# Optimization experiments

Hardware: AMD Instinct MI355X
Metric: run time of the kernel (lower is better)

The kernel has to match this reference:

```python
import jax, jax.numpy as jnp
import numpy as np

BATCH, N_IN, N_OUT, K = 32768, 256, 256, 8

def setup_inputs() -> dict:
    key = jax.random.key(0)
    k1, k2, k3 = jax.random.split(key, 3)
    x = jax.random.normal(k1, (BATCH, N_IN), dtype=jnp.float32)
    coef_a = jax.random.normal(k2, (N_OUT, N_IN, K), dtype=jnp.float32)
    coef_b = jax.random.normal(k3, (N_OUT, N_IN, K), dtype=jnp.float32)
    return {"x": x, "coef_a": coef_a, "coef_b": coef_b}

def reference(x, coef_a, coef_b):
    # Each edge (j, i) applies a univariate Fourier series to x[:, i]:
    #   f_ji(t) = sum_k a[j,i,k] * cos((k+1) t) + b[j,i,k] * sin((k+1) t)
    # Output: S[b, j] = sum_i f_ji(x[b, i])  (activation = identity)
    freqs = jnp.arange(1, K + 1, dtype=x.dtype)          # [K]
    phase = x[:, :, None] * freqs                        # [batch, n_in, K]
    S = (jnp.einsum('bik,jik->bj', jnp.cos(phase), coef_a)
         + jnp.einsum('bik,jik->bj', jnp.sin(phase), coef_b))
    return S
```

## Files before the change

### kernel.cpp

```cpp
#include <hip/hip_runtime.h>
#include <hip/hip_bf16.h>


#define NT 64

typedef __attribute__((ext_vector_type(8)))  short short8;
typedef __attribute__((ext_vector_type(16))) float f32x16;

typedef __attribute__((address_space(3))) void lds_void;
typedef const __attribute__((address_space(1))) void gbl_void;

static __device__ __forceinline__ unsigned short f2bf(float f) {
    union { float f; unsigned u; } v; v.f = f;
    unsigned r = v.u + 0x7fff + ((v.u >> 16) & 1);
    return (unsigned short)(r >> 16);
}

__global__ __launch_bounds__(256) void pack_w_kernel(
        const float* __restrict__ ca, const float* __restrict__ cb,
        unsigned short* __restrict__ wt) {
    int idx = blockIdx.x * 256 + threadIdx.x;
    int l  = idx & 63;
    int cg = (idx >> 6) & 7;
    int i  = idx >> 9;
    int j  = cg * 32 + (l & 31);
    const float* src = ((l >> 5) ? cb : ca) + ((size_t)j * 256 + i) * 8;
    float4 v0 = ((const float4*)src)[0];
    float4 v1 = ((const float4*)src)[1];
    alignas(16) unsigned short o[8];
    o[0] = f2bf(v0.x); o[1] = f2bf(v0.y); o[2] = f2bf(v0.z); o[3] = f2bf(v0.w);
    o[4] = f2bf(v1.x); o[5] = f2bf(v1.y); o[6] = f2bf(v1.z); o[7] = f2bf(v1.w);
    *(short8*)(wt + (size_t)idx * 8) = *(short8*)o;
}

template<bool PACKED>
__global__ __launch_bounds__(512, 2) void kan_gemm(
        const float* __restrict__ x,
        const unsigned short* __restrict__ bwt,
        const float* __restrict__ ca, const float* __restrict__ cb,
        float* __restrict__ out) {
    __shared__ __align__(16) char Alds[2][8][128][16];
    __shared__ __align__(16) char Blds[3][32768];

    const int tid   = threadIdx.x;
    const int l     = tid & 63;
    const int w     = tid >> 6;
    const int lrow  = l & 31;
    const int lhalf = l >> 5;
    const int wm    = w & 1;
    const int wn    = w >> 1;
    const int bm0   = blockIdx.x * 128;

    const int crow = tid >> 2;
    const int cii  = tid & 3;
    const float* xq = x + (size_t)(bm0 + crow) * 256 + cii;

    f32x16 acc[2][2];
#pragma unroll
    for (int m = 0; m < 2; ++m)
#pragma unroll
        for (int n = 0; n < 2; ++n)
#pragma unroll
            for (int r = 0; r < 16; ++r) acc[m][n][r] = 0.0f;

    auto stageB = [&](int dbuf, int tt) {
        if (PACKED) {
            const char* src = (const char*)bwt + (size_t)tt * 32768;
            char* dst = &Blds[dbuf][0];
#pragma unroll
            for (int p = 0; p < 4; ++p) {
                const int go = p * 512 + w * 64;
                __builtin_amdgcn_global_load_lds(
                    (gbl_void*)(src + (size_t)(go + l) * 16),
                    (lds_void*)(dst + (size_t)go * 16), 16, 0, 0);
            }
        } else {
#pragma unroll
            for (int p = 0; p < 4; ++p) {
                const int i = tt * 4 + p;
                const int j = w * 32 + lrow;
                const float* s = (lhalf ? cb : ca) + ((size_t)j * 256 + i) * 8;
                float4 v0 = ((const float4*)s)[0];
                float4 v1 = ((const float4*)s)[1];
                alignas(16) unsigned short o[8];
                o[0] = f2bf(v0.x); o[1] = f2bf(v0.y);
                o[2] = f2bf(v0.z); o[3] = f2bf(v0.w);
                o[4] = f2bf(v1.x); o[5] = f2bf(v1.y);
                o[6] = f2bf(v1.z); o[7] = f2bf(v1.w);
                *(short8*)(&Blds[dbuf][0] + (size_t)(p * 512 + w * 64 + l) * 16)
                    = *(short8*)o;
            }
        }
    };

    auto chains = [&](int abuf, float xv) {
        float s1, c1;
        __sincosf(xv, &s1, &c1);
        alignas(16) __hip_bfloat16 fc[8], fs[8];
        fc[0] = __float2bfloat16(c1); fs[0] = __float2bfloat16(s1);
        const float tc = c1 + c1;
        float cp2 = 1.0f, cp1 = c1, sp2 = 0.0f, sp1 = s1;
#pragma unroll
        for (int k = 1; k < 8; ++k) {
            const float cn = __builtin_fmaf(tc, cp1, -cp2);
            const float sn = __builtin_fmaf(tc, sp1, -sp2);
            cp2 = cp1; cp1 = cn; sp2 = sp1; sp1 = sn;
            fc[k] = __float2bfloat16(cn); fs[k] = __float2bfloat16(sn);
        }
        *(short8*)(&Alds[abuf][cii * 2 + 0][crow][0]) = *(short8*)fc;
        *(short8*)(&Alds[abuf][cii * 2 + 1][crow][0]) = *(short8*)fs;
    };

    float xcur  = xq[0];
    float xnext = xq[4];
    stageB(0, 0);
    float xnn   = xq[8];
    stageB(1, 1);
    chains(0, xcur);

    int rb = 0;
#pragma unroll 1
    for (int t = 0; t < NT; ++t) {
        __builtin_amdgcn_sched_barrier(0);
        asm volatile("s_waitcnt vmcnt(5) lgkmcnt(0)" ::: "memory");
        __builtin_amdgcn_s_barrier();
        __builtin_amdgcn_sched_barrier(0);

        const int tp2 = (t + 2 < NT) ? t + 2 : NT - 1;
        const int tp3 = (t + 3 < NT) ? t + 3 : NT - 1;
        const int sbuf = (rb + 2 >= 3) ? (rb - 1) : (rb + 2);

        const float xf = xq[(size_t)tp3 * 4];
        stageB(sbuf, tp2);

        chains((t + 1) & 1, xnext);

        const char* Ab = &Alds[t & 1][0][0][0];
        const char* Bb = &Blds[rb][0];
#pragma unroll
        for (int s = 0; s < 4; ++s) {
            const short8 a0 = *(const short8*)(
                Ab + (size_t)((s * 2 + lhalf) * 128 + wm * 64 + lrow) * 16);
            const short8 a1 = *(const short8*)(
                Ab + (size_t)((s * 2 + lhalf) * 128 + wm * 64 + 32 + lrow) * 16);
            const short8 b0 = *(const short8*)(
                Bb + (size_t)((s * 8 + wn * 2) * 64 + l) * 16);
            const short8 b1 = *(const short8*)(
                Bb + (size_t)((s * 8 + wn * 2 + 1) * 64 + l) * 16);
            __builtin_amdgcn_s_setprio(1);
            acc[0][0] = __builtin_amdgcn_mfma_f32_32x32x16_bf16(
                a0, b0, acc[0][0], 0, 0, 0);
            acc[0][1] = __builtin_amdgcn_mfma_f32_32x32x16_bf16(
                a0, b1, acc[0][1], 0, 0, 0);
            acc[1][0] = __builtin_amdgcn_mfma_f32_32x32x16_bf16(
                a1, b0, acc[1][0], 0, 0, 0);
            acc[1][1] = __builtin_amdgcn_mfma_f32_32x32x16_bf16(
                a1, b1, acc[1][1], 0, 0, 0);
            __builtin_amdgcn_s_setprio(0);
        }

        xnext = xnn; xnn = xf;
        rb = (rb + 1 == 3) ? 0 : rb + 1;
    }

#pragma unroll
    for (int m = 0; m < 2; ++m)
#pragma unroll
        for (int n = 0; n < 2; ++n) {
            const int ocol = wn * 64 + n * 32 + lrow;
#pragma unroll
            for (int r = 0; r < 16; ++r) {
                const int orow = bm0 + wm * 64 + m * 32
                               + (r & 3) + 8 * (r >> 2) + 4 * lhalf;
                out[(size_t)orow * 256 + ocol] = acc[m][n][r];
            }
        }
}

extern "C" void kernel_launch(void* const* d_in, const int* in_sizes, int n_in,
                              void* d_out, int out_size, void* d_ws, size_t ws_size,
                              hipStream_t stream) {
    const float* x  = (const float*)d_in[0];
    const float* ca = (const float*)d_in[1];
    const float* cb = (const float*)d_in[2];
    float* out = (float*)d_out;

    const size_t wt_bytes = (size_t)131072 * 16;

    if (ws_size >= wt_bytes) {
        unsigned short* wt = (unsigned short*)d_ws;
        pack_w_kernel<<<512, 256, 0, stream>>>(ca, cb, wt);
        kan_gemm<true><<<256, 512, 0, stream>>>(x, wt, ca, cb, out);
    } else {
        kan_gemm<false><<<256, 512, 0, stream>>>(x, nullptr, ca, cb, out);
    }
}
```

Before: 96.09 us.

## Split output columns across two blocks per row tile to double grid size

Each block now computes a 128x128 output tile (half the columns) instead of 128x256, and the grid doubles to 512 blocks. The B staging buffer is halved, the accumulators drop from four to two MFMA tiles, and launch bounds request four blocks per CU. The aim is better CU coverage and occupancy on a GPU with many CUs. The cost is that each block repeats the sin/cos feature generation for its rows, so that transcendental work is duplicated across the two column halves.

```diff
diff --git a/kernel.cpp b/kernel.cpp
--- a/kernel.cpp
+++ b/kernel.cpp
@@ -34,13 +34,13 @@
 }
 
 template<bool PACKED>
-__global__ __launch_bounds__(512, 2) void kan_gemm(
+__global__ __launch_bounds__(512, 4) void kan_gemm(
         const float* __restrict__ x,
         const unsigned short* __restrict__ bwt,
         const float* __restrict__ ca, const float* __restrict__ cb,
         float* __restrict__ out) {
     __shared__ __align__(16) char Alds[2][8][128][16];
-    __shared__ __align__(16) char Blds[3][32768];
+    __shared__ __align__(16) char Blds[3][16384];
 
     const int tid   = threadIdx.x;
     const int l     = tid & 63;
@@ -49,46 +49,45 @@
     const int lhalf = l >> 5;
     const int wm    = w & 1;
     const int wn    = w >> 1;
-    const int bm0   = blockIdx.x * 128;
+    const int rb    = blockIdx.x >> 1;
+    const int ch    = blockIdx.x & 1;
+    const int bm0   = rb * 128;
 
-    const int crow = tid >> 2;
-    const int cii  = tid & 3;
+    const int crow = tid & 127;
+    const int cii  = tid >> 7;
     const float* xq = x + (size_t)(bm0 + crow) * 256 + cii;
 
-    f32x16 acc[2][2];
+    f32x16 acc[2];
 #pragma unroll
     for (int m = 0; m < 2; ++m)
 #pragma unroll
-        for (int n = 0; n < 2; ++n)
-#pragma unroll
-            for (int r = 0; r < 16; ++r) acc[m][n][r] = 0.0f;
+        for (int r = 0; r < 16; ++r) acc[m][r] = 0.0f;
 
     auto stageB = [&](int dbuf, int tt) {
-        if (PACKED) {
-            const char* src = (const char*)bwt + (size_t)tt * 32768;
-            char* dst = &Blds[dbuf][0];
 #pragma unroll
-            for (int p = 0; p < 4; ++p) {
-                const int go = p * 512 + w * 64;
-                __builtin_amdgcn_global_load_lds(
-                    (gbl_void*)(src + (size_t)(go + l) * 16),
-                    (lds_void*)(dst + (size_t)go * 16), 16, 0, 0);
-            }
-        } else {
-#pragma unroll
-            for (int p = 0; p < 4; ++p) {
-                const int i = tt * 4 + p;
-                const int j = w * 32 + lrow;
-                const float* s = (lhalf ? cb : ca) + ((size_t)j * 256 + i) * 8;
-                float4 v0 = ((const float4*)s)[0];
-                float4 v1 = ((const float4*)s)[1];
+        for (int p = 0; p < 2; ++p) {
+            const int go = p * 512 + w * 64;
+            const int G  = (go + l) >> 6;
+            const int s  = G >> 2;
+            const int cgl = G & 3;
+            if (PACKED) {
+                const char* src = (const char*)bwt
+                    + ((size_t)(((tt * 4 + s) * 8 + ch * 4 + cgl) * 64 + l)) * 16;
+                char* dst = &Blds[dbuf][0] + (size_t)go * 16;
+                __builtin_amdgcn_global_load_lds((gbl_void*)src, (lds_void*)dst,
+                                                 16, 0, 0);
+            } else {
+                const int j = (ch * 4 + cgl) * 32 + lrow;
+                const int i = tt * 4 + s;
+                const float* sp = (lhalf ? cb : ca) + ((size_t)j * 256 + i) * 8;
+                float4 v0 = ((const float4*)sp)[0];
+                float4 v1 = ((const float4*)sp)[1];
                 alignas(16) unsigned short o[8];
                 o[0] = f2bf(v0.x); o[1] = f2bf(v0.y);
                 o[2] = f2bf(v0.z); o[3] = f2bf(v0.w);
                 o[4] = f2bf(v1.x); o[5] = f2bf(v1.y);
                 o[6] = f2bf(v1.z); o[7] = f2bf(v1.w);
-                *(short8*)(&Blds[dbuf][0] + (size_t)(p * 512 + w * 64 + l) * 16)
-                    = *(short8*)o;
+                *(short8*)(&Blds[dbuf][0] + (size_t)(go + l) * 16) = *(short8*)o;
             }
         }
     };
@@ -118,17 +117,17 @@
     stageB(1, 1);
     chains(0, xcur);
 
-    int rb = 0;
+    int rb3 = 0;
 #pragma unroll 1
     for (int t = 0; t < NT; ++t) {
         __builtin_amdgcn_sched_barrier(0);
-        asm volatile("s_waitcnt vmcnt(5) lgkmcnt(0)" ::: "memory");
+        asm volatile("s_waitcnt vmcnt(3) lgkmcnt(0)" ::: "memory");
         __builtin_amdgcn_s_barrier();
         __builtin_amdgcn_sched_barrier(0);
 
         const int tp2 = (t + 2 < NT) ? t + 2 : NT - 1;
         const int tp3 = (t + 3 < NT) ? t + 3 : NT - 1;
-        const int sbuf = (rb + 2 >= 3) ? (rb - 1) : (rb + 2);
+        const int sbuf = (rb3 + 2 >= 3) ? (rb3 - 1) : (rb3 + 2);
 
         const float xf = xq[(size_t)tp3 * 4];
         stageB(sbuf, tp2);
@@ -136,7 +135,7 @@
         chains((t + 1) & 1, xnext);
 
         const char* Ab = &Alds[t & 1][0][0][0];
-        const char* Bb = &Blds[rb][0];
+        const char* Bb = &Blds[rb3][0];
 #pragma unroll
         for (int s = 0; s < 4; ++s) {
             const short8 a0 = *(const short8*)(
@@ -144,36 +143,27 @@
             const short8 a1 = *(const short8*)(
                 Ab + (size_t)((s * 2 + lhalf) * 128 + wm * 64 + 32 + lrow) * 16);
             const short8 b0 = *(const short8*)(
-                Bb + (size_t)((s * 8 + wn * 2) * 64 + l) * 16);
-            const short8 b1 = *(const short8*)(
-                Bb + (size_t)((s * 8 + wn * 2 + 1) * 64 + l) * 16);
+                Bb + (size_t)((s * 4 + wn) * 64 + l) * 16);
             __builtin_amdgcn_s_setprio(1);
-            acc[0][0] = __builtin_amdgcn_mfma_f32_32x32x16_bf16(
-                a0, b0, acc[0][0], 0, 0, 0);
-            acc[0][1] = __builtin_amdgcn_mfma_f32_32x32x16_bf16(
-                a0, b1, acc[0][1], 0, 0, 0);
-            acc[1][0] = __builtin_amdgcn_mfma_f32_32x32x16_bf16(
-                a1, b0, acc[1][0], 0, 0, 0);
-            acc[1][1] = __builtin_amdgcn_mfma_f32_32x32x16_bf16(
-                a1, b1, acc[1][1], 0, 0, 0);
+            acc[0] = __builtin_amdgcn_mfma_f32_32x32x16_bf16(
+                a0, b0, acc[0], 0, 0, 0);
+            acc[1] = __builtin_amdgcn_mfma_f32_32x32x16_bf16(
+                a1, b0, acc[1], 0, 0, 0);
             __builtin_amdgcn_s_setprio(0);
         }
 
         xnext = xnn; xnn = xf;
-        rb = (rb + 1 == 3) ? 0 : rb + 1;
+        rb3 = (rb3 + 1 == 3) ? 0 : rb3 + 1;
     }
 
+    const int ocol = ch * 128 + wn * 32 + lrow;
 #pragma unroll
     for (int m = 0; m < 2; ++m)
 #pragma unroll
-        for (int n = 0; n < 2; ++n) {
-            const int ocol = wn * 64 + n * 32 + lrow;
-#pragma unroll
-            for (int r = 0; r < 16; ++r) {
-                const int orow = bm0 + wm * 64 + m * 32
-                               + (r & 3) + 8 * (r >> 2) + 4 * lhalf;
-                out[(size_t)orow * 256 + ocol] = acc[m][n][r];
-            }
+        for (int r = 0; r < 16; ++r) {
+            const int orow = bm0 + wm * 64 + m * 32
+                           + (r & 3) + 8 * (r >> 2) + 4 * lhalf;
+            out[(size_t)orow * 256 + ocol] = acc[m][r];
         }
 }
 
@@ -190,8 +180,8 @@
     if (ws_size >= wt_bytes) {
         unsigned short* wt = (unsigned short*)d_ws;
         pack_w_kernel<<<512, 256, 0, stream>>>(ca, cb, wt);
-        kan_gemm<true><<<256, 512, 0, stream>>>(x, wt, ca, cb, out);
+        kan_gemm<true><<<512, 512, 0, stream>>>(x, wt, ca, cb, out);
     } else {
-        kan_gemm<false><<<256, 512, 0, stream>>>(x, nullptr, ca, cb, out);
+        kan_gemm<false><<<512, 512, 0, stream>>>(x, nullptr, ca, cb, out);
     }
 }
```

Result: no change. 95.51 us (-0.6%).
